# Kernel tuning notes

Measured on AMD Instinct MI355X. Metric: run time of the kernel, lower is better.

## Reference

```python
import jax, jax.numpy as jnp
import numpy as np

B, S, D_IN, D_OUT = 4, 4096, 2048, 2048
NUM_ADAPTERS, RANK = 8, 16


def setup_inputs() -> dict:
    key = jax.random.key(0)
    ks = jax.random.split(key, 7)
    x = jax.random.normal(ks[0], (B, S, D_IN), dtype=jnp.float32)
    # adapter ids per token in [0, NUM_ADAPTERS]; 0 means 'no adapter'
    lora_mapping = jax.random.randint(ks[1], (B * S,), 0, NUM_ADAPTERS + 1, dtype=jnp.int32)
    weight = jax.random.normal(ks[2], (D_OUT, D_IN), dtype=jnp.float32) * (D_IN ** -0.5)
    bias = jax.random.normal(ks[3], (D_OUT,), dtype=jnp.float32) * 0.01
    # stacked adapters: aid a (1-indexed in mapping) lives at row a-1
    lora_a = jax.random.normal(ks[4], (NUM_ADAPTERS, RANK, D_IN), dtype=jnp.float32) * (D_IN ** -0.5)
    lora_b = jax.random.normal(ks[5], (NUM_ADAPTERS, D_OUT, RANK), dtype=jnp.float32) * (RANK ** -0.5)
    scaling = jnp.full((NUM_ADAPTERS,), 2.0, dtype=jnp.float32)
    return {"x": x, "lora_mapping": lora_mapping, "weight": weight, "bias": bias,
            "lora_a": lora_a, "lora_b": lora_b, "scaling": scaling}


def reference(x, lora_mapping, weight, bias, lora_a, lora_b, scaling):
    # Base dense linear: res = x @ W^T + b
    res = jnp.einsum('bsd,od->bso', x, weight) + bias  # [B,S,D_OUT]
    n_adapters = lora_a.shape[0]
    x2 = x.reshape(-1, x.shape[-1])                    # [N, D_IN]
    # one_hot(aid-1): aid==0 maps to -1 -> all-zero row (adapter skipped),
    # matching the torch loop that ignores aid 0. Fold scaling in here.
    sel = jax.nn.one_hot(lora_mapping - 1, n_adapters, dtype=x.dtype) * scaling  # [N, A]
    # Batched gather-matmul-scatter expressed as dense-over-adapters einsum:
    # u[n,a,r] = x[n] @ la[a]^T ; masked/scaled by sel ; delta[n] = sum_a u[n,a] @ lb[a]^T
    u = jnp.einsum('nd,ard->nar', x2, lora_a) * sel[..., None]  # [N, A, R]
    delta = jnp.einsum('nar,aor->no', u, lora_b)                # [N, D_OUT]
    return res + delta.reshape(res.shape)
```

## Files before the change

kernel.cpp:

```cpp
#include <hip/hip_runtime.h>
#include <hip/hip_bf16.h>


#define D_IN   2048
#define D_OUT  2048
#define NTOK   16384
#define RANK   16
#define NADAPT 8
#define KEXT   2176
#define BM     128
#define BN     128
#define BK     64
#define EBM    32
#define EBK    128

typedef __attribute__((ext_vector_type(8))) __bf16 bf16x8;
typedef __attribute__((ext_vector_type(8))) unsigned short u16x8;
typedef __attribute__((ext_vector_type(4))) float  f32x4;

__device__ inline unsigned short f2bf(float f) {
    unsigned u = __builtin_bit_cast(unsigned, f);
    u += 0x7fffu + ((u >> 16) & 1u);
    return (unsigned short)(u >> 16);
}

#define SEG0 ((size_t)NTOK * 256)
#define SEG1 (SEG0 + (size_t)D_OUT * 256)
#define SEG2 (SEG1 + 32768)
#define TOTU (SEG2 + 32768)
#define CONV_SPAN 598016

__global__ void conv_prep(const float* __restrict__ x, const float* __restrict__ w,
                          const float* __restrict__ la, const float* __restrict__ lb,
                          unsigned short* __restrict__ Xe, unsigned short* __restrict__ We,
                          unsigned short* __restrict__ La) {
    size_t gid = (size_t)blockIdx.x * 256 + threadIdx.x;
    float4 v0[8], v1[8];
    unsigned short* dst[8];
#pragma unroll
    for (int j = 0; j < 8; ++j) {
        size_t u = (size_t)j * CONV_SPAN + gid;
        const float* src;
        unsigned short* d;
        if (u < SEG0) {
            int n = (int)(u >> 8), kc = ((int)u & 255) * 8;
            src = x + (size_t)n * D_IN + kc;
            d   = Xe + (size_t)n * KEXT + kc;
        } else if (u < SEG1) {
            size_t v = u - SEG0;
            int o = (int)(v >> 8), kc = ((int)v & 255) * 8;
            src = w + (size_t)o * D_IN + kc;
            d   = We + (size_t)o * KEXT + kc;
        } else if (u < SEG2) {
            size_t v = u - SEG1;
            src = la + v * 8;
            d   = La + v * 8;
        } else {
            size_t v = u - SEG2;
            int o = (int)(v >> 4), m = (int)v & 15;
            int a = m >> 1, r = (m & 1) * 8;
            src = lb + ((size_t)a * D_OUT + o) * RANK + r;
            d   = We + (size_t)o * KEXT + D_IN + m * 8;
        }
        v0[j] = *(const float4*)(src);
        v1[j] = *(const float4*)(src + 4);
        dst[j] = d;
    }
#pragma unroll
    for (int j = 0; j < 8; ++j) {
        u16x8 s;
        s[0] = f2bf(v0[j].x); s[1] = f2bf(v0[j].y); s[2] = f2bf(v0[j].z); s[3] = f2bf(v0[j].w);
        s[4] = f2bf(v1[j].x); s[5] = f2bf(v1[j].y); s[6] = f2bf(v1[j].z); s[7] = f2bf(v1[j].w);
        *(u16x8*)dst[j] = s;
    }
}

__global__ void ext_gemm(unsigned short* Xe, const int* __restrict__ map,
                         const unsigned short* __restrict__ La,
                         const float* __restrict__ scaling) {
    __shared__ unsigned short As[2][EBM * EBK];
    __shared__ unsigned short Bs[2][128 * EBK];

    int t = threadIdx.x, lane = t & 63, wave = t >> 6;
    int n0 = blockIdx.x * EBM;

    f32x4 acc[2][2] = {};

    auto stage = [&](int buf, int kt) {
        int k0 = kt * EBK;
#pragma unroll
        for (int c = 0; c < 2; ++c) {
            int linear = (wave * 2 + c) * 64 + lane;
            int row = linear >> 4, kc = linear & 15;
            int gc = kc ^ (row & 7);
            const unsigned short* ga = Xe + (size_t)(n0 + row) * KEXT + k0 + gc * 8;
            __builtin_amdgcn_global_load_lds(
                (const __attribute__((address_space(1))) unsigned int*)ga,
                (__attribute__((address_space(3))) unsigned int*)(&As[buf][0] + (wave * 2 + c) * 512),
                16, 0, 0);
        }
#pragma unroll
        for (int c = 0; c < 8; ++c) {
            int linear = (wave * 8 + c) * 64 + lane;
            int row = linear >> 4, kc = linear & 15;
            int gc = kc ^ (row & 7);
            const unsigned short* gb = La + (size_t)row * D_IN + k0 + gc * 8;
            __builtin_amdgcn_global_load_lds(
                (const __attribute__((address_space(1))) unsigned int*)gb,
                (__attribute__((address_space(3))) unsigned int*)(&Bs[buf][0] + (wave * 8 + c) * 512),
                16, 0, 0);
        }
    };

    auto compute = [&](int buf) {
#pragma unroll
        for (int ks = 0; ks < 4; ++ks) {
            int gchunk = ks * 4 + (lane >> 4);
            int sw = gchunk ^ (lane & 7);
            bf16x8 af[2], bfr[2];
#pragma unroll
            for (int i = 0; i < 2; ++i)
                af[i] = *(const bf16x8*)(&As[buf][(i * 16 + (lane & 15)) * EBK + sw * 8]);
#pragma unroll
            for (int j = 0; j < 2; ++j)
                bfr[j] = *(const bf16x8*)(&Bs[buf][(wave * 32 + j * 16 + (lane & 15)) * EBK + sw * 8]);
#pragma unroll
            for (int i = 0; i < 2; ++i)
#pragma unroll
                for (int j = 0; j < 2; ++j)
                    acc[i][j] = __builtin_amdgcn_mfma_f32_16x16x32_bf16(af[i], bfr[j], acc[i][j], 0, 0, 0);
        }
    };

    stage(0, 0);
    __syncthreads();
    int cur = 0;
    for (int kt = 0; kt < D_IN / EBK; ++kt) {
        if (kt + 1 < D_IN / EBK) stage(cur ^ 1, kt + 1);
        compute(cur);
        __syncthreads();
        cur ^= 1;
    }

    int colq = lane & 15, rq = lane >> 4;
#pragma unroll
    for (int j = 0; j < 2; ++j) {
        int c = wave * 32 + j * 16 + colq;
        int aid = wave * 2 + j + 1;
        float sc = scaling[wave * 2 + j];
#pragma unroll
        for (int i = 0; i < 2; ++i) {
#pragma unroll
            for (int r = 0; r < 4; ++r) {
                int token = n0 + i * 16 + rq * 4 + r;
                unsigned short v = 0;
                if (map[token] == aid) v = f2bf(acc[i][j][r] * sc);
                Xe[(size_t)token * KEXT + D_IN + c] = v;
            }
        }
    }
}

__global__ void gemm_fused(const unsigned short* __restrict__ Xe,
                           const unsigned short* __restrict__ We,
                           const float* __restrict__ bias,
                           float* __restrict__ out) {
    __shared__ unsigned short As[BM * BK];
    __shared__ unsigned short Bs[BN * BK];

    int t = threadIdx.x;
    int lane = t & 63, wave = t >> 6;
    int g = blockIdx.x;
    int group = g >> 7, within = g & 127;
    int bm = group * 8 + (within & 7);
    int bn = within >> 3;

    int wm = wave >> 1, wn = wave & 1;
    f32x4 acc[4][4] = {};

    for (int k0 = 0; k0 < KEXT; k0 += BK) {
        __syncthreads();
#pragma unroll
        for (int c = 0; c < 4; ++c) {
            int linear = (wave * 4 + c) * 64 + lane;
            int row = linear >> 3;
            int kc  = linear & 7;
            int gc  = kc ^ (row & 7);
            const unsigned short* ga = Xe + (size_t)(bm * BM + row) * KEXT + k0 + gc * 8;
            __builtin_amdgcn_global_load_lds(
                (const __attribute__((address_space(1))) unsigned int*)ga,
                (__attribute__((address_space(3))) unsigned int*)(As + (wave * 4 + c) * 512),
                16, 0, 0);
            const unsigned short* gb = We + (size_t)(bn * BN + row) * KEXT + k0 + gc * 8;
            __builtin_amdgcn_global_load_lds(
                (const __attribute__((address_space(1))) unsigned int*)gb,
                (__attribute__((address_space(3))) unsigned int*)(Bs + (wave * 4 + c) * 512),
                16, 0, 0);
        }
        __syncthreads();
#pragma unroll
        for (int ks = 0; ks < 2; ++ks) {
            bf16x8 af[4], bfr[4];
            int gchunk = ks * 4 + (lane >> 4);
            int sw = gchunk ^ (lane & 7);
#pragma unroll
            for (int i = 0; i < 4; ++i) {
                int rowA = wm * 64 + i * 16 + (lane & 15);
                af[i]  = *(const bf16x8*)(As + rowA * BK + sw * 8);
                int rowB = wn * 64 + i * 16 + (lane & 15);
                bfr[i] = *(const bf16x8*)(Bs + rowB * BK + sw * 8);
            }
#pragma unroll
            for (int i = 0; i < 4; ++i)
#pragma unroll
                for (int j = 0; j < 4; ++j)
                    acc[i][j] = __builtin_amdgcn_mfma_f32_16x16x32_bf16(af[i], bfr[j], acc[i][j], 0, 0, 0);
        }
    }

    int colq = lane & 15, rq = lane >> 4;
#pragma unroll
    for (int j = 0; j < 4; ++j) {
        int col = bn * BN + wn * 64 + j * 16 + colq;
        float bv = bias[col];
#pragma unroll
        for (int i = 0; i < 4; ++i) {
            int row0 = bm * BM + wm * 64 + i * 16 + rq * 4;
#pragma unroll
            for (int r = 0; r < 4; ++r)
                out[(size_t)(row0 + r) * D_OUT + col] = acc[i][j][r] + bv;
        }
    }
}

extern "C" void kernel_launch(void* const* d_in, const int* in_sizes, int n_in,
                              void* d_out, int out_size, void* d_ws, size_t ws_size,
                              hipStream_t stream) {
    (void)in_sizes; (void)n_in; (void)out_size; (void)ws_size;
    const float* x       = (const float*)d_in[0];
    const int*   map     = (const int*)d_in[1];
    const float* weight  = (const float*)d_in[2];
    const float* bias    = (const float*)d_in[3];
    const float* lora_a  = (const float*)d_in[4];
    const float* lora_b  = (const float*)d_in[5];
    const float* scaling = (const float*)d_in[6];
    float* out = (float*)d_out;

    unsigned short* Xe = (unsigned short*)d_ws;
    unsigned short* We = Xe + (size_t)NTOK * KEXT;
    unsigned short* La = We + (size_t)D_OUT * KEXT;

    conv_prep<<<2336, 256, 0, stream>>>(x, weight, lora_a, lora_b, Xe, We, La);
    ext_gemm<<<NTOK / EBM, 256, 0, stream>>>(Xe, map, La, scaling);
    gemm_fused<<<(NTOK / BM) * (D_OUT / BN), 256, 0, stream>>>(Xe, We, bias, out);
}
```

Baseline: 403.3 us.

## Fuse input conversion with LoRA-A projection and remap GEMM block order

Merges the fp32-to-bf16 conversion of x and lora_a into the LoRA-A projection kernel. Each token block now converts its x rows in registers, writes them to the extended activation buffer and to shared memory, and runs the MFMA projection from there. This removes one launch and the re-read of the bf16 activations from global memory. Weight and lora_b conversion run in extra blocks of the same launch. The main GEMM also gets a block-index permutation that interleaves tiles across groups, likely for XCD/L2 locality. In exchange, the fused kernel reloads and reconverts the lora_a tile in every block and drops the double-buffered async LDS staging.

```diff
diff --git a/kernel.cpp b/kernel.cpp
--- a/kernel.cpp
+++ b/kernel.cpp
@@ -11,8 +11,6 @@
 #define BM     128
 #define BN     128
 #define BK     64
-#define EBM    32
-#define EBK    128
 
 typedef __attribute__((ext_vector_type(8))) __bf16 bf16x8;
 typedef __attribute__((ext_vector_type(8))) unsigned short u16x8;
@@ -24,122 +22,124 @@
     return (unsigned short)(u >> 16);
 }
 
-#define SEG0 ((size_t)NTOK * 256)
-#define SEG1 (SEG0 + (size_t)D_OUT * 256)
-#define SEG2 (SEG1 + 32768)
-#define TOTU (SEG2 + 32768)
-#define CONV_SPAN 598016
-
-__global__ void conv_prep(const float* __restrict__ x, const float* __restrict__ w,
-                          const float* __restrict__ la, const float* __restrict__ lb,
-                          unsigned short* __restrict__ Xe, unsigned short* __restrict__ We,
-                          unsigned short* __restrict__ La) {
-    size_t gid = (size_t)blockIdx.x * 256 + threadIdx.x;
-    float4 v0[8], v1[8];
-    unsigned short* dst[8];
+__device__ inline u16x8 cvt8(float4 a, float4 b) {
+    u16x8 s;
+    s[0] = f2bf(a.x); s[1] = f2bf(a.y); s[2] = f2bf(a.z); s[3] = f2bf(a.w);
+    s[4] = f2bf(b.x); s[5] = f2bf(b.y); s[6] = f2bf(b.z); s[7] = f2bf(b.w);
+    return s;
+}
+
+__global__ void prep_fused(const float* __restrict__ x, const float* __restrict__ w,
+                           const float* __restrict__ la, const float* __restrict__ lb,
+                           const int* __restrict__ map, const float* __restrict__ scaling,
+                           unsigned short* __restrict__ Xe, unsigned short* __restrict__ We) {
+    __shared__ unsigned short Xb[32 * 128];
+    __shared__ unsigned short Lat[128 * 128];
+
+    int t = threadIdx.x;
+
+    if (blockIdx.x >= 512) {
+        int gid = (blockIdx.x - 512) * 256 + t;
+        float4 v0[8], v1[8];
+        unsigned short* dst[8];
+#pragma unroll
+        for (int j = 0; j < 8; ++j) {
+            int u = j * 69632 + gid;
+            const float* src;
+            unsigned short* d;
+            if (u < 524288) {
+                int o = u >> 8, kc = (u & 255) * 8;
+                src = w + (size_t)o * D_IN + kc;
+                d   = We + (size_t)o * KEXT + kc;
+            } else {
+                int v = u - 524288;
+                int o = v >> 4, m = v & 15;
+                int a = m >> 1, r = (m & 1) * 8;
+                src = lb + ((size_t)a * D_OUT + o) * RANK + r;
+                d   = We + (size_t)o * KEXT + D_IN + m * 8;
+            }
+            v0[j] = *(const float4*)src;
+            v1[j] = *(const float4*)(src + 4);
+            dst[j] = d;
+        }
+#pragma unroll
+        for (int j = 0; j < 8; ++j)
+            *(u16x8*)dst[j] = cvt8(v0[j], v1[j]);
+        return;
+    }
+
+    int lane = t & 63, wave = t >> 6;
+    int n0 = blockIdx.x * 32;
+
+    f32x4 acc[2][2] = {};
+    float4 xv[4];
+    float4 lv[16];
+
+#pragma unroll
+    for (int s2 = 0; s2 < 2; ++s2) {
+        int s = t + s2 * 256, row = s >> 4, ch = s & 15;
+        const float* src = x + (size_t)(n0 + row) * D_IN + ch * 8;
+        xv[s2 * 2] = *(const float4*)src;
+        xv[s2 * 2 + 1] = *(const float4*)(src + 4);
+    }
 #pragma unroll
     for (int j = 0; j < 8; ++j) {
-        size_t u = (size_t)j * CONV_SPAN + gid;
-        const float* src;
-        unsigned short* d;
-        if (u < SEG0) {
-            int n = (int)(u >> 8), kc = ((int)u & 255) * 8;
-            src = x + (size_t)n * D_IN + kc;
-            d   = Xe + (size_t)n * KEXT + kc;
-        } else if (u < SEG1) {
-            size_t v = u - SEG0;
-            int o = (int)(v >> 8), kc = ((int)v & 255) * 8;
-            src = w + (size_t)o * D_IN + kc;
-            d   = We + (size_t)o * KEXT + kc;
-        } else if (u < SEG2) {
-            size_t v = u - SEG1;
-            src = la + v * 8;
-            d   = La + v * 8;
-        } else {
-            size_t v = u - SEG2;
-            int o = (int)(v >> 4), m = (int)v & 15;
-            int a = m >> 1, r = (m & 1) * 8;
-            src = lb + ((size_t)a * D_OUT + o) * RANK + r;
-            d   = We + (size_t)o * KEXT + D_IN + m * 8;
-        }
-        v0[j] = *(const float4*)(src);
-        v1[j] = *(const float4*)(src + 4);
-        dst[j] = d;
-    }
-#pragma unroll
-    for (int j = 0; j < 8; ++j) {
-        u16x8 s;
-        s[0] = f2bf(v0[j].x); s[1] = f2bf(v0[j].y); s[2] = f2bf(v0[j].z); s[3] = f2bf(v0[j].w);
-        s[4] = f2bf(v1[j].x); s[5] = f2bf(v1[j].y); s[6] = f2bf(v1[j].z); s[7] = f2bf(v1[j].w);
-        *(u16x8*)dst[j] = s;
-    }
-}
-
-__global__ void ext_gemm(unsigned short* Xe, const int* __restrict__ map,
-                         const unsigned short* __restrict__ La,
-                         const float* __restrict__ scaling) {
-    __shared__ unsigned short As[2][EBM * EBK];
-    __shared__ unsigned short Bs[2][128 * EBK];
-
-    int t = threadIdx.x, lane = t & 63, wave = t >> 6;
-    int n0 = blockIdx.x * EBM;
-
-    f32x4 acc[2][2] = {};
-
-    auto stage = [&](int buf, int kt) {
-        int k0 = kt * EBK;
-#pragma unroll
-        for (int c = 0; c < 2; ++c) {
-            int linear = (wave * 2 + c) * 64 + lane;
-            int row = linear >> 4, kc = linear & 15;
-            int gc = kc ^ (row & 7);
-            const unsigned short* ga = Xe + (size_t)(n0 + row) * KEXT + k0 + gc * 8;
-            __builtin_amdgcn_global_load_lds(
-                (const __attribute__((address_space(1))) unsigned int*)ga,
-                (__attribute__((address_space(3))) unsigned int*)(&As[buf][0] + (wave * 2 + c) * 512),
-                16, 0, 0);
-        }
-#pragma unroll
-        for (int c = 0; c < 8; ++c) {
-            int linear = (wave * 8 + c) * 64 + lane;
-            int row = linear >> 4, kc = linear & 15;
-            int gc = kc ^ (row & 7);
-            const unsigned short* gb = La + (size_t)row * D_IN + k0 + gc * 8;
-            __builtin_amdgcn_global_load_lds(
-                (const __attribute__((address_space(1))) unsigned int*)gb,
-                (__attribute__((address_space(3))) unsigned int*)(&Bs[buf][0] + (wave * 8 + c) * 512),
-                16, 0, 0);
-        }
-    };
-
-    auto compute = [&](int buf) {
+        int s = t + j * 256, c = s >> 4, ch = s & 15;
+        const float* src = la + (size_t)c * D_IN + ch * 8;
+        lv[j * 2] = *(const float4*)src;
+        lv[j * 2 + 1] = *(const float4*)(src + 4);
+    }
+
+    for (int kt = 0; kt < 16; ++kt) {
+        int k0 = kt * 128;
+        __syncthreads();
+#pragma unroll
+        for (int s2 = 0; s2 < 2; ++s2) {
+            int s = t + s2 * 256, row = s >> 4, ch = s & 15;
+            u16x8 o = cvt8(xv[s2 * 2], xv[s2 * 2 + 1]);
+            *(u16x8*)(Xe + (size_t)(n0 + row) * KEXT + k0 + ch * 8) = o;
+            *(u16x8*)(Xb + row * 128 + (ch ^ (row & 7)) * 8) = o;
+        }
+#pragma unroll
+        for (int j = 0; j < 8; ++j) {
+            int s = t + j * 256, c = s >> 4, ch = s & 15;
+            *(u16x8*)(Lat + c * 128 + (ch ^ (c & 7)) * 8) = cvt8(lv[j * 2], lv[j * 2 + 1]);
+        }
+        if (kt < 15) {
+            int k1 = k0 + 128;
+#pragma unroll
+            for (int s2 = 0; s2 < 2; ++s2) {
+                int s = t + s2 * 256, row = s >> 4, ch = s & 15;
+                const float* src = x + (size_t)(n0 + row) * D_IN + k1 + ch * 8;
+                xv[s2 * 2] = *(const float4*)src;
+                xv[s2 * 2 + 1] = *(const float4*)(src + 4);
+            }
+#pragma unroll
+            for (int j = 0; j < 8; ++j) {
+                int s = t + j * 256, c = s >> 4, ch = s & 15;
+                const float* src = la + (size_t)c * D_IN + k1 + ch * 8;
+                lv[j * 2] = *(const float4*)src;
+                lv[j * 2 + 1] = *(const float4*)(src + 4);
+            }
+        }
+        __syncthreads();
 #pragma unroll
         for (int ks = 0; ks < 4; ++ks) {
-            int gchunk = ks * 4 + (lane >> 4);
-            int sw = gchunk ^ (lane & 7);
+            int chunk = ks * 4 + (lane >> 4);
+            int sw = chunk ^ (lane & 7);
             bf16x8 af[2], bfr[2];
 #pragma unroll
             for (int i = 0; i < 2; ++i)
-                af[i] = *(const bf16x8*)(&As[buf][(i * 16 + (lane & 15)) * EBK + sw * 8]);
+                af[i] = *(const bf16x8*)(Xb + (i * 16 + (lane & 15)) * 128 + sw * 8);
 #pragma unroll
             for (int j = 0; j < 2; ++j)
-                bfr[j] = *(const bf16x8*)(&Bs[buf][(wave * 32 + j * 16 + (lane & 15)) * EBK + sw * 8]);
+                bfr[j] = *(const bf16x8*)(Lat + (wave * 32 + j * 16 + (lane & 15)) * 128 + sw * 8);
 #pragma unroll
             for (int i = 0; i < 2; ++i)
 #pragma unroll
                 for (int j = 0; j < 2; ++j)
                     acc[i][j] = __builtin_amdgcn_mfma_f32_16x16x32_bf16(af[i], bfr[j], acc[i][j], 0, 0, 0);
         }
-    };
-
-    stage(0, 0);
-    __syncthreads();
-    int cur = 0;
-    for (int kt = 0; kt < D_IN / EBK; ++kt) {
-        if (kt + 1 < D_IN / EBK) stage(cur ^ 1, kt + 1);
-        compute(cur);
-        __syncthreads();
-        cur ^= 1;
     }
 
     int colq = lane & 15, rq = lane >> 4;
@@ -170,7 +170,8 @@
 
     int t = threadIdx.x;
     int lane = t & 63, wave = t >> 6;
-    int g = blockIdx.x;
+    int gb = blockIdx.x;
+    int g = (gb & 7) * 256 + (gb >> 3);
     int group = g >> 7, within = g & 127;
     int bm = group * 8 + (within & 7);
     int bn = within >> 3;
@@ -191,9 +192,9 @@
                 (const __attribute__((address_space(1))) unsigned int*)ga,
                 (__attribute__((address_space(3))) unsigned int*)(As + (wave * 4 + c) * 512),
                 16, 0, 0);
-            const unsigned short* gb = We + (size_t)(bn * BN + row) * KEXT + k0 + gc * 8;
+            const unsigned short* gb2 = We + (size_t)(bn * BN + row) * KEXT + k0 + gc * 8;
             __builtin_amdgcn_global_load_lds(
-                (const __attribute__((address_space(1))) unsigned int*)gb,
+                (const __attribute__((address_space(1))) unsigned int*)gb2,
                 (__attribute__((address_space(3))) unsigned int*)(Bs + (wave * 4 + c) * 512),
                 16, 0, 0);
         }
@@ -248,9 +249,7 @@
 
     unsigned short* Xe = (unsigned short*)d_ws;
     unsigned short* We = Xe + (size_t)NTOK * KEXT;
-    unsigned short* La = We + (size_t)D_OUT * KEXT;
-
-    conv_prep<<<2336, 256, 0, stream>>>(x, weight, lora_a, lora_b, Xe, We, La);
-    ext_gemm<<<NTOK / EBM, 256, 0, stream>>>(Xe, map, La, scaling);
+
+    prep_fused<<<784, 256, 0, stream>>>(x, weight, lora_a, lora_b, map, scaling, Xe, We);
     gemm_fused<<<(NTOK / BM) * (D_OUT / BN), 256, 0, stream>>>(Xe, We, bias, out);
 }
```

Result: slower. 470.9 us (+16.8%).

## Split conversion kernel and remap GEMM tiles so each XCD owns fixed N columns

Applied to the files above, without the earlier changes.

The fused conversion kernel, where each thread handled 8 strided elements across segments, is replaced by two simple kernels: one converting x with one 8-element chunk per thread, and one converting the weights and adapters. The main GEMM block-to-tile mapping changes so that blocks landing on the same XCD (blockIdx mod 8) share two fixed BN column tiles of the weight, aiming to improve per-XCD L2 reuse of We. The cost is an extra kernel launch and a different pattern of reuse for the A tiles across XCDs.

```diff
diff --git a/kernel.cpp b/kernel.cpp
--- a/kernel.cpp
+++ b/kernel.cpp
@@ -24,55 +24,46 @@
     return (unsigned short)(u >> 16);
 }
 
-#define SEG0 ((size_t)NTOK * 256)
-#define SEG1 (SEG0 + (size_t)D_OUT * 256)
-#define SEG2 (SEG1 + 32768)
-#define TOTU (SEG2 + 32768)
-#define CONV_SPAN 598016
-
-__global__ void conv_prep(const float* __restrict__ x, const float* __restrict__ w,
-                          const float* __restrict__ la, const float* __restrict__ lb,
-                          unsigned short* __restrict__ Xe, unsigned short* __restrict__ We,
-                          unsigned short* __restrict__ La) {
-    size_t gid = (size_t)blockIdx.x * 256 + threadIdx.x;
-    float4 v0[8], v1[8];
-    unsigned short* dst[8];
-#pragma unroll
-    for (int j = 0; j < 8; ++j) {
-        size_t u = (size_t)j * CONV_SPAN + gid;
-        const float* src;
-        unsigned short* d;
-        if (u < SEG0) {
-            int n = (int)(u >> 8), kc = ((int)u & 255) * 8;
-            src = x + (size_t)n * D_IN + kc;
-            d   = Xe + (size_t)n * KEXT + kc;
-        } else if (u < SEG1) {
-            size_t v = u - SEG0;
-            int o = (int)(v >> 8), kc = ((int)v & 255) * 8;
-            src = w + (size_t)o * D_IN + kc;
-            d   = We + (size_t)o * KEXT + kc;
-        } else if (u < SEG2) {
-            size_t v = u - SEG1;
-            src = la + v * 8;
-            d   = La + v * 8;
-        } else {
-            size_t v = u - SEG2;
-            int o = (int)(v >> 4), m = (int)v & 15;
-            int a = m >> 1, r = (m & 1) * 8;
-            src = lb + ((size_t)a * D_OUT + o) * RANK + r;
-            d   = We + (size_t)o * KEXT + D_IN + m * 8;
-        }
-        v0[j] = *(const float4*)(src);
-        v1[j] = *(const float4*)(src + 4);
-        dst[j] = d;
-    }
-#pragma unroll
-    for (int j = 0; j < 8; ++j) {
-        u16x8 s;
-        s[0] = f2bf(v0[j].x); s[1] = f2bf(v0[j].y); s[2] = f2bf(v0[j].z); s[3] = f2bf(v0[j].w);
-        s[4] = f2bf(v1[j].x); s[5] = f2bf(v1[j].y); s[6] = f2bf(v1[j].z); s[7] = f2bf(v1[j].w);
-        *(u16x8*)dst[j] = s;
-    }
+__device__ inline u16x8 cvt8(float4 a, float4 b) {
+    u16x8 s;
+    s[0] = f2bf(a.x); s[1] = f2bf(a.y); s[2] = f2bf(a.z); s[3] = f2bf(a.w);
+    s[4] = f2bf(b.x); s[5] = f2bf(b.y); s[6] = f2bf(b.z); s[7] = f2bf(b.w);
+    return s;
+}
+
+__global__ void conv_x(const float* __restrict__ x, unsigned short* __restrict__ Xe) {
+    int t = blockIdx.x * 256 + threadIdx.x;
+    int n = t >> 8, kc = (t & 255) * 8;
+    const float* src = x + (size_t)n * D_IN + kc;
+    float4 v0 = *(const float4*)src;
+    float4 v1 = *(const float4*)(src + 4);
+    *(u16x8*)(Xe + (size_t)n * KEXT + kc) = cvt8(v0, v1);
+}
+
+__global__ void conv_w(const float* __restrict__ w, const float* __restrict__ la,
+                       const float* __restrict__ lb,
+                       unsigned short* __restrict__ We, unsigned short* __restrict__ La) {
+    int u = blockIdx.x * 256 + threadIdx.x;
+    const float* src;
+    unsigned short* dst;
+    if (u < 524288) {
+        int o = u >> 8, kc = (u & 255) * 8;
+        src = w + (size_t)o * D_IN + kc;
+        dst = We + (size_t)o * KEXT + kc;
+    } else if (u < 557056) {
+        int v = u - 524288;
+        src = la + (size_t)v * 8;
+        dst = La + (size_t)v * 8;
+    } else {
+        int v = u - 557056;
+        int o = v >> 4, m = v & 15;
+        int a = m >> 1, r = (m & 1) * 8;
+        src = lb + ((size_t)a * D_OUT + o) * RANK + r;
+        dst = We + (size_t)o * KEXT + D_IN + m * 8;
+    }
+    float4 v0 = *(const float4*)src;
+    float4 v1 = *(const float4*)(src + 4);
+    *(u16x8*)dst = cvt8(v0, v1);
 }
 
 __global__ void ext_gemm(unsigned short* Xe, const int* __restrict__ map,
@@ -170,10 +161,10 @@
 
     int t = threadIdx.x;
     int lane = t & 63, wave = t >> 6;
-    int g = blockIdx.x;
-    int group = g >> 7, within = g & 127;
-    int bm = group * 8 + (within & 7);
-    int bn = within >> 3;
+    int gb = blockIdx.x;
+    int xcd = gb & 7, idx = gb >> 3;
+    int bm = idx >> 1;
+    int bn = xcd * 2 + (idx & 1);
 
     int wm = wave >> 1, wn = wave & 1;
     f32x4 acc[4][4] = {};
@@ -191,9 +182,9 @@
                 (const __attribute__((address_space(1))) unsigned int*)ga,
                 (__attribute__((address_space(3))) unsigned int*)(As + (wave * 4 + c) * 512),
                 16, 0, 0);
-            const unsigned short* gb = We + (size_t)(bn * BN + row) * KEXT + k0 + gc * 8;
-            __builtin_amdgcn_global_load_lds(
-                (const __attribute__((address_space(1))) unsigned int*)gb,
+            const unsigned short* gb2 = We + (size_t)(bn * BN + row) * KEXT + k0 + gc * 8;
+            __builtin_amdgcn_global_load_lds(
+                (const __attribute__((address_space(1))) unsigned int*)gb2,
                 (__attribute__((address_space(3))) unsigned int*)(Bs + (wave * 4 + c) * 512),
                 16, 0, 0);
         }
@@ -250,7 +241,8 @@
     unsigned short* We = Xe + (size_t)NTOK * KEXT;
     unsigned short* La = We + (size_t)D_OUT * KEXT;
 
-    conv_prep<<<2336, 256, 0, stream>>>(x, weight, lora_a, lora_b, Xe, We, La);
+    conv_x<<<NTOK, 256, 0, stream>>>(x, Xe);
+    conv_w<<<2304, 256, 0, stream>>>(weight, lora_a, lora_b, We, La);
     ext_gemm<<<NTOK / EBM, 256, 0, stream>>>(Xe, map, La, scaling);
     gemm_fused<<<(NTOK / BM) * (D_OUT / BN), 256, 0, stream>>>(Xe, We, bias, out);
 }
```

Measured after the change: 405.7 us. About the same (+0.6%).
